# Kernel optimization log

Measured on AMD Instinct MI355X. Metric: run time of the kernel, lower is better.

The kernel has to match this reference:

```python
import jax, jax.numpy as jnp
import numpy as np

B, TQ, TKV, D, H = 4, 512, 4096, 1024, 8
HEAD_DIM = D // H


def setup_inputs() -> dict:
    key = jax.random.key(0)
    ks = jax.random.split(key, 8)
    s = 0.02
    inputs_q = jax.random.normal(ks[0], (B, TQ, D), jnp.float32)
    inputs_kv = jax.random.normal(ks[1], (B, TKV, D), jnp.float32)
    attention_mask = jax.random.randint(ks[2], (B, TQ, TKV), 0, 2).astype(bool)
    Wq = jax.random.normal(ks[3], (D, D), jnp.float32) * s
    Wk = jax.random.normal(ks[4], (D, D), jnp.float32) * s
    Wv = jax.random.normal(ks[5], (D, D), jnp.float32) * s
    Wo = jax.random.normal(ks[6], (D, D), jnp.float32) * s
    zb = jnp.zeros((D,), jnp.float32)
    return {"inputs_q": inputs_q, "inputs_kv": inputs_kv, "attention_mask": attention_mask,
            "Wq": Wq, "bq": zb, "Wk": Wk, "bk": zb, "Wv": Wv, "bv": zb, "Wo": Wo, "bo": zb}


def _split_heads(x, h):
    b, t, c = x.shape
    return x.reshape(b, t, h, c // h).transpose(0, 2, 1, 3)  # b h t d


def reference(inputs_q, inputs_kv, attention_mask, Wq, bq, Wk, bk, Wv, bv, Wo, bo):
    q = _split_heads(inputs_q @ Wq + bq, H)   # [b,h,tq,d]
    k = _split_heads(inputs_kv @ Wk + bk, H)  # [b,h,tkv,d]
    v = _split_heads(inputs_kv @ Wv + bv, H)  # [b,h,tkv,d]
    scale = 1.0 / np.sqrt(HEAD_DIM).astype(np.float32)
    scores = jnp.einsum('bhtd,bhTd->bhtT', q, k) * scale
    large_k = jnp.asarray(1e30, scores.dtype)  # 1e30 for fp32 per source
    scores = jnp.where(attention_mask[:, None, :, :], scores, -large_k)
    probs = jax.nn.softmax(scores, axis=-1)
    summed = jnp.einsum('bhtT,bhTd->bhtd', probs, v)
    b, h, t, d = summed.shape
    summed = summed.transpose(0, 2, 1, 3).reshape(b, t, h * d)  # [b,tq,hiddens]
    # wipe rows whose mask is entirely zero (post-softmax wipe-masking)
    wipe = jnp.all(~attention_mask, axis=-1, keepdims=True)  # [b,tq,1]
    summed = jnp.where(wipe, jnp.zeros_like(summed), summed)
    return summed @ Wo + bo
```

## Files before the change

kernel.cpp:

```cpp
#include <hip/hip_runtime.h>
#include <cstdint>
#include <cstddef>

typedef unsigned short US;
typedef __bf16 bf16_t;
typedef bf16_t bf16x8 __attribute__((ext_vector_type(8)));
typedef float  f32x4  __attribute__((ext_vector_type(4)));
typedef US     us8    __attribute__((ext_vector_type(8)));
typedef US     us4    __attribute__((ext_vector_type(4)));

#define AS1 __attribute__((address_space(1)))
#define AS3 __attribute__((address_space(3)))

__device__ __forceinline__ void gl_lds16(const void* g, void* l) {
    __builtin_amdgcn_global_load_lds((AS1 unsigned int*)(size_t)g,
                                     (AS3 unsigned int*)l, 16, 0, 0);
}

__device__ __forceinline__ US f2bf(float f) {
    unsigned u = __builtin_bit_cast(unsigned, f);
    u += 0x7FFFu + ((u >> 16) & 1u);
    return (US)(u >> 16);
}

__device__ __forceinline__ bf16x8 ldv8(const US* p) {
    return __builtin_bit_cast(bf16x8, *(const us8*)p);
}

__global__ void prep(const float* __restrict__ Xq, const float* __restrict__ Xkv,
                     const int* __restrict__ Mi, US* __restrict__ XqB,
                     US* __restrict__ XkvB, unsigned long long* __restrict__ MBits) {
    int b = blockIdx.x, tid = threadIdx.x;
    if (b < 2048) {
        int i = b * 256 + tid;
        float4 f = ((const float4*)Xq)[i];
        us4 o = { f2bf(f.x), f2bf(f.y), f2bf(f.z), f2bf(f.w) };
        ((us4*)XqB)[i] = o;
    } else if (b < 18432) {
        int i = (b - 2048) * 256 + tid;
        float4 f = ((const float4*)Xkv)[i];
        us4 o = { f2bf(f.x), f2bf(f.y), f2bf(f.z), f2bf(f.w) };
        ((us4*)XkvB)[i] = o;
    } else {
        int i = (b - 18432) * 256 + tid;
        int m = Mi[i];
        unsigned long long bits = __ballot(m != 0);
        if ((tid & 63) == 0) MBits[i >> 6] = bits;
    }
}

__global__ void wt_conv(const float* __restrict__ Wq, const float* __restrict__ Wk,
                        const float* __restrict__ Wv, const float* __restrict__ Wo,
                        US* __restrict__ outbase) {
    const float* W = (blockIdx.z == 0) ? Wq : (blockIdx.z == 1) ? Wk
                   : (blockIdx.z == 2) ? Wv : Wo;
    US* WT = outbase + (size_t)blockIdx.z * 1024 * 1024;
    __shared__ float t[32][33];
    int tx = threadIdx.x & 31, ty = threadIdx.x >> 5;
    int x = blockIdx.x * 32 + tx;
#pragma unroll
    for (int r = 0; r < 4; ++r)
        t[ty + r * 8][tx] = W[(size_t)(blockIdx.y * 32 + ty + r * 8) * 1024 + x];
    __syncthreads();
    int nx = blockIdx.y * 32 + tx;
#pragma unroll
    for (int r = 0; r < 4; ++r)
        WT[(size_t)(blockIdx.x * 32 + ty + r * 8) * 1024 + nx] = f2bf(t[tx][ty + r * 8]);
}

template <int MODE, int BM>
__global__ __launch_bounds__(256, 2)
void gemm_bt(const US* __restrict__ A, const US* __restrict__ Bt,
             const float* __restrict__ bias, void* __restrict__ out,
             int tlog2, float scale) {
    constexpr int K = 1024, N = 1024, BK = 64;
    constexpr int MI = BM / 32;
    __shared__ US As[BM * BK];
    __shared__ US Bs[128 * BK];
    const int tid = threadIdx.x;
    const int wv = tid >> 6, ln = tid & 63;
    const int g = ln >> 4, c15 = ln & 15;
    const int m0 = blockIdx.x * BM, n0 = blockIdx.y * 128;
    const int wm = (wv & 1) * (BM / 2), wn = (wv >> 1) * 64;

    f32x4 acc[MI][4];
    const f32x4 z = {0.f, 0.f, 0.f, 0.f};
#pragma unroll
    for (int i = 0; i < MI; ++i)
#pragma unroll
        for (int j = 0; j < 4; ++j) acc[i][j] = z;

    const US* Ab = A + (size_t)m0 * K;
    const US* Bb = Bt + (size_t)n0 * K;

    for (int k0 = 0; k0 < K; k0 += BK) {
        __syncthreads();
#pragma unroll
        for (int q = 0; q < BM / 32; ++q) {
            int eb = (q * 256 + wv * 64) * 8;
            int r = (eb >> 6) + (ln >> 3);
            int sw = (ln & 7) ^ (r & 7);
            gl_lds16(Ab + (size_t)r * K + k0 + sw * 8, &As[eb]);
        }
#pragma unroll
        for (int q = 0; q < 4; ++q) {
            int eb = (q * 256 + wv * 64) * 8;
            int r = (eb >> 6) + (ln >> 3);
            int sw = (ln & 7) ^ (r & 7);
            gl_lds16(Bb + (size_t)r * K + k0 + sw * 8, &Bs[eb]);
        }
        __syncthreads();
#pragma unroll
        for (int ks = 0; ks < 2; ++ks) {
            bf16x8 a[MI], b[4];
#pragma unroll
            for (int i = 0; i < MI; ++i) {
                int p = (ks * 4 + g) ^ (c15 & 7);
                a[i] = ldv8(&As[(wm + i * 16 + c15) * BK + p * 8]);
            }
#pragma unroll
            for (int j = 0; j < 4; ++j) {
                int p = (ks * 4 + g) ^ (c15 & 7);
                b[j] = ldv8(&Bs[(wn + j * 16 + c15) * BK + p * 8]);
            }
#pragma unroll
            for (int i = 0; i < MI; ++i)
#pragma unroll
                for (int j = 0; j < 4; ++j)
                    acc[i][j] = __builtin_amdgcn_mfma_f32_16x16x32_bf16(a[i], b[j], acc[i][j], 0, 0, 0);
        }
    }

#pragma unroll
    for (int i = 0; i < MI; ++i) {
#pragma unroll
        for (int j = 0; j < 4; ++j) {
            int col = n0 + wn + j * 16 + c15;
            float bvv = bias[col];
#pragma unroll
            for (int r = 0; r < 4; ++r) {
                int row = m0 + wm + i * 16 + g * 4 + r;
                float v = (acc[i][j][r] + bvv) * scale;
                if (MODE == 0) {
                    int b_ = row >> tlog2;
                    int t = row & ((1 << tlog2) - 1);
                    int h = col >> 7, d = col & 127;
                    ((US*)out)[(((size_t)(b_ * 8 + h) << tlog2) + t) * 128 + d] = f2bf(v);
                } else {
                    ((float*)out)[(size_t)row * N + col] = v;
                }
            }
        }
    }
}

__global__ __launch_bounds__(256, 2)
void gemm_kv(const US* __restrict__ A, const US* __restrict__ BtK,
             const US* __restrict__ BtV, const float* __restrict__ bk,
             const float* __restrict__ bv, US* __restrict__ Kout,
             US* __restrict__ VTout) {
    constexpr int K = 1024, BK = 64;
    __shared__ US lds[3 * 128 * BK];
    US* As  = lds;
    US* BsK = lds + 128 * BK;
    US* BsV = lds + 2 * 128 * BK;
    const int tid = threadIdx.x;
    const int wv = tid >> 6, ln = tid & 63;
    const int g = ln >> 4, c15 = ln & 15;
    const int m0 = blockIdx.x * 128, n0 = blockIdx.y * 128;
    const int wm = (wv & 1) * 64, wn = (wv >> 1) * 64;

    f32x4 aK[4][4], aV[4][4];
    const f32x4 z = {0.f, 0.f, 0.f, 0.f};
#pragma unroll
    for (int i = 0; i < 4; ++i)
#pragma unroll
        for (int j = 0; j < 4; ++j) { aK[i][j] = z; aV[i][j] = z; }

    const US* Ab  = A   + (size_t)m0 * K;
    const US* BbK = BtK + (size_t)n0 * K;
    const US* BbV = BtV + (size_t)n0 * K;

    for (int k0 = 0; k0 < K; k0 += BK) {
        __syncthreads();
#pragma unroll
        for (int q = 0; q < 4; ++q) {
            int eb = (q * 256 + wv * 64) * 8;
            int r = (eb >> 6) + (ln >> 3);
            int sw = (ln & 7) ^ (r & 7);
            gl_lds16(Ab  + (size_t)r * K + k0 + sw * 8, &As[eb]);
            gl_lds16(BbK + (size_t)r * K + k0 + sw * 8, &BsK[eb]);
            gl_lds16(BbV + (size_t)r * K + k0 + sw * 8, &BsV[eb]);
        }
        __syncthreads();
#pragma unroll
        for (int ks = 0; ks < 2; ++ks) {
            bf16x8 a[4], bK[4], bV[4];
#pragma unroll
            for (int i = 0; i < 4; ++i) {
                int p = (ks * 4 + g) ^ (c15 & 7);
                a[i] = ldv8(&As[(wm + i * 16 + c15) * BK + p * 8]);
            }
#pragma unroll
            for (int j = 0; j < 4; ++j) {
                int p = (ks * 4 + g) ^ (c15 & 7);
                bK[j] = ldv8(&BsK[(wn + j * 16 + c15) * BK + p * 8]);
                bV[j] = ldv8(&BsV[(wn + j * 16 + c15) * BK + p * 8]);
            }
#pragma unroll
            for (int i = 0; i < 4; ++i)
#pragma unroll
                for (int j = 0; j < 4; ++j) {
                    aK[i][j] = __builtin_amdgcn_mfma_f32_16x16x32_bf16(a[i], bK[j], aK[i][j], 0, 0, 0);
                    aV[i][j] = __builtin_amdgcn_mfma_f32_16x16x32_bf16(a[i], bV[j], aV[i][j], 0, 0, 0);
                }
        }
    }

    const int h = n0 >> 7;
    const int b_ = m0 >> 12, tbase = m0 & 4095;

#pragma unroll
    for (int i = 0; i < 4; ++i) {
#pragma unroll
        for (int j = 0; j < 4; ++j) {
            int col = n0 + wn + j * 16 + c15;
            float bkv = bk[col];
            int d = col & 127;
#pragma unroll
            for (int r = 0; r < 4; ++r) {
                int row = m0 + wm + i * 16 + g * 4 + r;
                int t = row & 4095;
                Kout[(((size_t)(b_ * 8 + h) << 12) + t) * 128 + d] = f2bf(aK[i][j][r] + bkv);
            }
        }
    }

    __syncthreads();
    US* T = lds;
#pragma unroll
    for (int i = 0; i < 4; ++i) {
#pragma unroll
        for (int j = 0; j < 4; ++j) {
            int dcol = wn + j * 16 + c15;
            float bvv = bv[n0 + dcol];
#pragma unroll
            for (int r = 0; r < 4; ++r) {
                int kvrow = wm + i * 16 + g * 4 + r;
                T[dcol * 136 + kvrow] = f2bf(aV[i][j][r] + bvv);
            }
        }
    }
    __syncthreads();
    {
        int d = tid >> 1, half = (tid & 1) * 64;
        US* vrow = VTout + ((size_t)(b_ * 8 + h) * 128 + d) * 4096 + tbase + half;
        const US* tr = &T[d * 136 + half];
#pragma unroll
        for (int s = 0; s < 8; ++s)
            *(us8*)(vrow + s * 8) = *(const us8*)(tr + s * 8);
    }
}

__global__ __launch_bounds__(256, 3)
void flash(const US* __restrict__ Qh, const US* __restrict__ Kh,
           const US* __restrict__ VTh, const unsigned long long* __restrict__ MBits,
           float* __restrict__ Opart, float* __restrict__ Lpart) {
    __shared__ US Ks[64 * 128];
    __shared__ US Vs[128 * 64];
    __shared__ US Ps[4][32 * 64];
    const int tid = threadIdx.x, wv = tid >> 6, ln = tid & 63;
    const int g = ln >> 4, c15 = ln & 15;
    const int qt = blockIdx.x, qbase = qt * 128;
    const int bh = blockIdx.y, b_ = bh >> 3;
    const int sp = blockIdx.z;
    const int t0 = (sp < 4) ? sp * 11 : 44 + (sp - 4) * 10;
    const int nt = (sp < 4) ? 11 : 10;
    const int wq = wv * 32;

    bf16x8 qa[2][4];
#pragma unroll
    for (int ib = 0; ib < 2; ++ib) {
        const US* qrow = Qh + ((size_t)bh * 512 + qbase + wq + ib * 16 + c15) * 128;
#pragma unroll
        for (int ks = 0; ks < 4; ++ks)
            qa[ib][ks] = ldv8(qrow + ks * 32 + g * 8);
    }

    f32x4 o[8][2];
    const f32x4 z = {0.f, 0.f, 0.f, 0.f};
#pragma unroll
    for (int d = 0; d < 8; ++d) { o[d][0] = z; o[d][1] = z; }
    float l2[2] = {0.f, 0.f};

    const unsigned long long* Mrow[2];
    Mrow[0] = MBits + (size_t)(b_ * 512 + qbase + wq + c15) * 64;
    Mrow[1] = Mrow[0] + (size_t)16 * 64;
    const US* Kbase = Kh + ((size_t)bh * 4096 + (size_t)t0 * 64) * 128;
    const US* Vbase = VTh + (size_t)bh * 128 * 4096;
    US* Pw = &Ps[wv][0];

    for (int t = 0; t < nt; ++t) {
        int kv0 = (t0 + t) * 64;
        __syncthreads();
        const US* Kb = Kbase + (size_t)t * 64 * 128;
#pragma unroll
        for (int q = 0; q < 4; ++q) {
            int eb = (q * 256 + wv * 64) * 8;
            int r = (eb >> 7) + (ln >> 4);
            int sw = (ln & 15) ^ (r & 15);
            gl_lds16(Kb + (size_t)r * 128 + sw * 8, &Ks[eb]);
        }
#pragma unroll
        for (int q = 0; q < 4; ++q) {
            int eb = (q * 256 + wv * 64) * 8;
            int r = (eb >> 6) + (ln >> 3);
            int sw = (ln & 7) ^ (r & 7);
            gl_lds16(Vbase + (size_t)r * 4096 + kv0 + sw * 8, &Vs[eb]);
        }
        unsigned long long m64[2];
        m64[0] = Mrow[0][t0 + t];
        m64[1] = Mrow[1][t0 + t];
        __syncthreads();

#pragma unroll
        for (int kb = 0; kb < 4; ++kb) {
            f32x4 s0 = z, s1 = z;
#pragma unroll
            for (int ks = 0; ks < 4; ++ks) {
                bf16x8 kf = ldv8(&Ks[(kb * 16 + c15) * 128 + (((ks * 4 + g) ^ c15) * 8)]);
                s0 = __builtin_amdgcn_mfma_f32_16x16x32_bf16(kf, qa[0][ks], s0, 0, 0, 0);
                s1 = __builtin_amdgcn_mfma_f32_16x16x32_bf16(kf, qa[1][ks], s1, 0, 0, 0);
            }
            int cw = kb * 4 + g;
#pragma unroll
            for (int ib = 0; ib < 2; ++ib) {
                f32x4 sv = ib ? s1 : s0;
                unsigned mq = (unsigned)(m64[ib] >> (kb * 16 + g * 4)) & 15u;
                float p0 = (mq & 1u) ? __expf(sv[0]) : 0.f;
                float p1 = (mq & 2u) ? __expf(sv[1]) : 0.f;
                float p2 = (mq & 4u) ? __expf(sv[2]) : 0.f;
                float p3 = (mq & 8u) ? __expf(sv[3]) : 0.f;
                l2[ib] += (p0 + p1) + (p2 + p3);
                int q = ib * 16 + c15;
                US* wp = Pw + q * 64 + (((cw >> 1) ^ (q & 7)) * 8) + (cw & 1) * 4;
                us4 pv = { f2bf(p0), f2bf(p1), f2bf(p2), f2bf(p3) };
                *(us4*)wp = pv;
            }
        }

#pragma unroll
        for (int ks = 0; ks < 2; ++ks) {
            bf16x8 pf[2];
#pragma unroll
            for (int ib = 0; ib < 2; ++ib) {
                int q = ib * 16 + c15;
                pf[ib] = ldv8(&Pw[q * 64 + (((ks * 4 + g) ^ (q & 7)) * 8)]);
            }
#pragma unroll
            for (int d = 0; d < 8; ++d) {
                bf16x8 vf = ldv8(&Vs[(d * 16 + c15) * 64 + (((ks * 4 + g) ^ (c15 & 7)) * 8)]);
                o[d][0] = __builtin_amdgcn_mfma_f32_16x16x32_bf16(vf, pf[0], o[d][0], 0, 0, 0);
                o[d][1] = __builtin_amdgcn_mfma_f32_16x16x32_bf16(vf, pf[1], o[d][1], 0, 0, 0);
            }
        }
    }

    float lf[2];
#pragma unroll
    for (int ib = 0; ib < 2; ++ib) {
        float l = l2[ib];
        l += __shfl_xor(l, 16); l += __shfl_xor(l, 32);
        lf[ib] = l;
    }
    if (ln < 16) {
        size_t lb = ((size_t)sp * 32 + bh) * 512 + qbase + wq + c15;
        Lpart[lb] = lf[0];
        Lpart[lb + 16] = lf[1];
    }
    float* Ob = Opart + (((size_t)sp * 32 + bh) * 128 + g * 4) * 512 + qbase + wq + c15;
#pragma unroll
    for (int d = 0; d < 8; ++d)
#pragma unroll
        for (int r = 0; r < 4; ++r) {
            Ob[(size_t)(d * 16 + r) * 512] = o[d][0][r];
            Ob[(size_t)(d * 16 + r) * 512 + 16] = o[d][1][r];
        }
}

__global__ void combine(const float* __restrict__ Opart, const float* __restrict__ Lpart,
                        US* __restrict__ AO) {
    __shared__ float linv[128];
    __shared__ float T[128 * 33];
    const int qt = blockIdx.x, bh = blockIdx.y;
    const int b_ = bh >> 3, h = bh & 7;
    const int tid = threadIdx.x;
    const size_t spstride = (size_t)32 * 128 * 512;

    if (tid < 128) {
        float s = 0.f;
#pragma unroll
        for (int sp = 0; sp < 6; ++sp)
            s += Lpart[((size_t)sp * 32 + bh) * 512 + qt * 128 + tid];
        linv[tid] = (s > 0.f) ? 1.f / s : 0.f;
    }
    __syncthreads();

    for (int ds0 = 0; ds0 < 128; ds0 += 32) {
        if (ds0) __syncthreads();
#pragma unroll
        for (int it = 0; it < 4; ++it) {
            int d = ds0 + (tid >> 5) + it * 8, qc = tid & 31;
            const float* base = Opart + ((size_t)bh * 128 + d) * 512 + qt * 128 + qc * 4;
            float4 a = {0.f, 0.f, 0.f, 0.f};
#pragma unroll
            for (int sp = 0; sp < 6; ++sp) {
                float4 v = *(const float4*)(base + sp * spstride);
                a.x += v.x; a.y += v.y; a.z += v.z; a.w += v.w;
            }
            int dd = d - ds0;
            T[(qc * 4 + 0) * 33 + dd] = a.x * linv[qc * 4 + 0];
            T[(qc * 4 + 1) * 33 + dd] = a.y * linv[qc * 4 + 1];
            T[(qc * 4 + 2) * 33 + dd] = a.z * linv[qc * 4 + 2];
            T[(qc * 4 + 3) * 33 + dd] = a.w * linv[qc * 4 + 3];
        }
        __syncthreads();
#pragma unroll
        for (int it = 0; it < 4; ++it) {
            int idx = tid + it * 256;
            int q = idx >> 3, c = idx & 7;
            const float* tr = &T[q * 33 + c * 4];
            us4 ov = { f2bf(tr[0]), f2bf(tr[1]), f2bf(tr[2]), f2bf(tr[3]) };
            *(us4*)(AO + ((size_t)(b_ * 512 + qt * 128 + q)) * 1024 + h * 128 + ds0 + c * 4) = ov;
        }
    }
}

extern "C" void kernel_launch(void* const* d_in, const int* in_sizes, int n_in,
                              void* d_out, int out_size, void* d_ws, size_t ws_size,
                              hipStream_t stream) {
    (void)in_sizes; (void)n_in; (void)out_size; (void)ws_size;
    const float* Xq  = (const float*)d_in[0];
    const float* Xkv = (const float*)d_in[1];
    const int*   Mi  = (const int*)d_in[2];
    const float* Wq  = (const float*)d_in[3];
    const float* bq  = (const float*)d_in[4];
    const float* Wk  = (const float*)d_in[5];
    const float* bk  = (const float*)d_in[6];
    const float* Wv  = (const float*)d_in[7];
    const float* bv  = (const float*)d_in[8];
    const float* Wo  = (const float*)d_in[9];
    const float* bo  = (const float*)d_in[10];
    float* out = (float*)d_out;

    char* p = (char*)d_ws;
    US* WT   = (US*)p; p += (size_t)4 * 1024 * 1024 * 2;
    US* AO   = (US*)p; p += (size_t)2048 * 1024 * 2;
    US* XqB  = (US*)p; p += (size_t)2048 * 1024 * 2;
    US* Qh   = (US*)p; p += (size_t)2048 * 1024 * 2;
    US* Kh   = (US*)p; p += (size_t)16384 * 1024 * 2;
    US* VTh  = (US*)p; p += (size_t)16384 * 1024 * 2;
    US* XkvB = (US*)p; p += (size_t)16384 * 1024 * 2;
    char* OT = p;      p += (size_t)4 * 1024 * 1024 * 4;
    unsigned long long* MBits = (unsigned long long*)p; p += (size_t)131072 * 8;
    (void)OT;
    float* Opart = (float*)XkvB;
    float* Lpart = (float*)XqB;

    prep<<<51200, 256, 0, stream>>>(Xq, Xkv, Mi, XqB, XkvB, MBits);
    wt_conv<<<dim3(32, 32, 4), 256, 0, stream>>>(Wq, Wk, Wv, Wo, WT);

    gemm_bt<0, 64><<<dim3(32, 8), 256, 0, stream>>>(XqB, WT, bq, Qh, 9, 0.08838834764831843f);
    gemm_kv<<<dim3(128, 8), 256, 0, stream>>>(XkvB, WT + 1048576, WT + 2097152,
                                              bk, bv, Kh, VTh);
    flash<<<dim3(4, 32, 6), 256, 0, stream>>>(Qh, Kh, VTh, MBits, Opart, Lpart);
    combine<<<dim3(4, 32), 256, 0, stream>>>(Opart, Lpart, AO);
    gemm_bt<1, 64><<<dim3(32, 8), 256, 0, stream>>>(AO, WT + 3145728, bo, out, 0, 1.0f);
}
```

Measured before the change: 351.9 us.

## Fuse weight conversion into prep, store flash partials as bf16, remap flash grid

New measurement: 344.1 us. -2.2%, faster.

```diff
diff --git a/kernel.cpp b/kernel.cpp
--- a/kernel.cpp
+++ b/kernel.cpp
@@ -23,13 +23,21 @@
     return (US)(u >> 16);
 }
 
+__device__ __forceinline__ float bf2f(US u) {
+    return __builtin_bit_cast(float, (unsigned)u << 16);
+}
+
 __device__ __forceinline__ bf16x8 ldv8(const US* p) {
     return __builtin_bit_cast(bf16x8, *(const us8*)p);
 }
 
 __global__ void prep(const float* __restrict__ Xq, const float* __restrict__ Xkv,
                      const int* __restrict__ Mi, US* __restrict__ XqB,
-                     US* __restrict__ XkvB, unsigned long long* __restrict__ MBits) {
+                     US* __restrict__ XkvB, unsigned long long* __restrict__ MBits,
+                     const float* __restrict__ Wq, const float* __restrict__ Wk,
+                     const float* __restrict__ Wv, const float* __restrict__ Wo,
+                     US* __restrict__ WTbase) {
+    __shared__ float t[32][33];
     int b = blockIdx.x, tid = threadIdx.x;
     if (b < 2048) {
         int i = b * 256 + tid;
@@ -41,31 +49,28 @@
         float4 f = ((const float4*)Xkv)[i];
         us4 o = { f2bf(f.x), f2bf(f.y), f2bf(f.z), f2bf(f.w) };
         ((us4*)XkvB)[i] = o;
-    } else {
+    } else if (b < 51200) {
         int i = (b - 18432) * 256 + tid;
         int m = Mi[i];
         unsigned long long bits = __ballot(m != 0);
         if ((tid & 63) == 0) MBits[i >> 6] = bits;
-    }
-}
-
-__global__ void wt_conv(const float* __restrict__ Wq, const float* __restrict__ Wk,
-                        const float* __restrict__ Wv, const float* __restrict__ Wo,
-                        US* __restrict__ outbase) {
-    const float* W = (blockIdx.z == 0) ? Wq : (blockIdx.z == 1) ? Wk
-                   : (blockIdx.z == 2) ? Wv : Wo;
-    US* WT = outbase + (size_t)blockIdx.z * 1024 * 1024;
-    __shared__ float t[32][33];
-    int tx = threadIdx.x & 31, ty = threadIdx.x >> 5;
-    int x = blockIdx.x * 32 + tx;
-#pragma unroll
-    for (int r = 0; r < 4; ++r)
-        t[ty + r * 8][tx] = W[(size_t)(blockIdx.y * 32 + ty + r * 8) * 1024 + x];
-    __syncthreads();
-    int nx = blockIdx.y * 32 + tx;
-#pragma unroll
-    for (int r = 0; r < 4; ++r)
-        WT[(size_t)(blockIdx.x * 32 + ty + r * 8) * 1024 + nx] = f2bf(t[tx][ty + r * 8]);
+    } else {
+        int wb = b - 51200;
+        int z = wb >> 10, rr = wb & 1023;
+        int bx = rr & 31, by = rr >> 5;
+        const float* W = (z == 0) ? Wq : (z == 1) ? Wk : (z == 2) ? Wv : Wo;
+        US* WT = WTbase + (size_t)z * 1024 * 1024;
+        int tx = tid & 31, ty = tid >> 5;
+        int x = bx * 32 + tx;
+#pragma unroll
+        for (int r = 0; r < 4; ++r)
+            t[ty + r * 8][tx] = W[(size_t)(by * 32 + ty + r * 8) * 1024 + x];
+        __syncthreads();
+        int nx = by * 32 + tx;
+#pragma unroll
+        for (int r = 0; r < 4; ++r)
+            WT[(size_t)(bx * 32 + ty + r * 8) * 1024 + nx] = f2bf(t[tx][ty + r * 8]);
+    }
 }
 
 template <int MODE, int BM>
@@ -265,15 +270,18 @@
 __global__ __launch_bounds__(256, 3)
 void flash(const US* __restrict__ Qh, const US* __restrict__ Kh,
            const US* __restrict__ VTh, const unsigned long long* __restrict__ MBits,
-           float* __restrict__ Opart, float* __restrict__ Lpart) {
+           US* __restrict__ Opart, float* __restrict__ Lpart) {
     __shared__ US Ks[64 * 128];
     __shared__ US Vs[128 * 64];
     __shared__ US Ps[4][32 * 64];
     const int tid = threadIdx.x, wv = tid >> 6, ln = tid & 63;
     const int g = ln >> 4, c15 = ln & 15;
-    const int qt = blockIdx.x, qbase = qt * 128;
-    const int bh = blockIdx.y, b_ = bh >> 3;
-    const int sp = blockIdx.z;
+    const int bid = blockIdx.x;
+    const int qt = bid / 192;
+    const int rest = bid - qt * 192;
+    const int bh = rest / 6, sp = rest - bh * 6;
+    const int qbase = qt * 128;
+    const int b_ = bh >> 3;
     const int t0 = (sp < 4) ? sp * 11 : 44 + (sp - 4) * 10;
     const int nt = (sp < 4) ? 11 : 10;
     const int wq = wv * 32;
@@ -378,17 +386,17 @@
         Lpart[lb] = lf[0];
         Lpart[lb + 16] = lf[1];
     }
-    float* Ob = Opart + (((size_t)sp * 32 + bh) * 128 + g * 4) * 512 + qbase + wq + c15;
+    US* Ob = Opart + (((size_t)sp * 32 + bh) * 128 + g * 4) * 512 + qbase + wq + c15;
 #pragma unroll
     for (int d = 0; d < 8; ++d)
 #pragma unroll
         for (int r = 0; r < 4; ++r) {
-            Ob[(size_t)(d * 16 + r) * 512] = o[d][0][r];
-            Ob[(size_t)(d * 16 + r) * 512 + 16] = o[d][1][r];
-        }
-}
-
-__global__ void combine(const float* __restrict__ Opart, const float* __restrict__ Lpart,
+            Ob[(size_t)(d * 16 + r) * 512] = f2bf(o[d][0][r]);
+            Ob[(size_t)(d * 16 + r) * 512 + 16] = f2bf(o[d][1][r]);
+        }
+}
+
+__global__ void combine(const US* __restrict__ Opart, const float* __restrict__ Lpart,
                         US* __restrict__ AO) {
     __shared__ float linv[128];
     __shared__ float T[128 * 33];
@@ -408,21 +416,27 @@
 
     for (int ds0 = 0; ds0 < 128; ds0 += 32) {
         if (ds0) __syncthreads();
-#pragma unroll
-        for (int it = 0; it < 4; ++it) {
-            int d = ds0 + (tid >> 5) + it * 8, qc = tid & 31;
-            const float* base = Opart + ((size_t)bh * 128 + d) * 512 + qt * 128 + qc * 4;
-            float4 a = {0.f, 0.f, 0.f, 0.f};
+        {
+            int d = ds0 + (tid >> 3);
+            int q0 = (tid & 7) * 16;
+            const US* base = Opart + ((size_t)bh * 128 + d) * 512 + qt * 128 + q0;
+            float acc[16];
+#pragma unroll
+            for (int i = 0; i < 16; ++i) acc[i] = 0.f;
 #pragma unroll
             for (int sp = 0; sp < 6; ++sp) {
-                float4 v = *(const float4*)(base + sp * spstride);
-                a.x += v.x; a.y += v.y; a.z += v.z; a.w += v.w;
+                us8 a = *(const us8*)(base + sp * spstride);
+                us8 b = *(const us8*)(base + sp * spstride + 8);
+#pragma unroll
+                for (int i = 0; i < 8; ++i) {
+                    acc[i] += bf2f(a[i]);
+                    acc[8 + i] += bf2f(b[i]);
+                }
             }
             int dd = d - ds0;
-            T[(qc * 4 + 0) * 33 + dd] = a.x * linv[qc * 4 + 0];
-            T[(qc * 4 + 1) * 33 + dd] = a.y * linv[qc * 4 + 1];
-            T[(qc * 4 + 2) * 33 + dd] = a.z * linv[qc * 4 + 2];
-            T[(qc * 4 + 3) * 33 + dd] = a.w * linv[qc * 4 + 3];
+#pragma unroll
+            for (int i = 0; i < 16; ++i)
+                T[(q0 + i) * 33 + dd] = acc[i] * linv[q0 + i];
         }
         __syncthreads();
 #pragma unroll
@@ -461,19 +475,16 @@
     US* Kh   = (US*)p; p += (size_t)16384 * 1024 * 2;
     US* VTh  = (US*)p; p += (size_t)16384 * 1024 * 2;
     US* XkvB = (US*)p; p += (size_t)16384 * 1024 * 2;
-    char* OT = p;      p += (size_t)4 * 1024 * 1024 * 4;
     unsigned long long* MBits = (unsigned long long*)p; p += (size_t)131072 * 8;
-    (void)OT;
-    float* Opart = (float*)XkvB;
+    US* Opart    = XkvB;
     float* Lpart = (float*)XqB;
 
-    prep<<<51200, 256, 0, stream>>>(Xq, Xkv, Mi, XqB, XkvB, MBits);
-    wt_conv<<<dim3(32, 32, 4), 256, 0, stream>>>(Wq, Wk, Wv, Wo, WT);
+    prep<<<55296, 256, 0, stream>>>(Xq, Xkv, Mi, XqB, XkvB, MBits, Wq, Wk, Wv, Wo, WT);
 
     gemm_bt<0, 64><<<dim3(32, 8), 256, 0, stream>>>(XqB, WT, bq, Qh, 9, 0.08838834764831843f);
     gemm_kv<<<dim3(128, 8), 256, 0, stream>>>(XkvB, WT + 1048576, WT + 2097152,
                                               bk, bv, Kh, VTh);
-    flash<<<dim3(4, 32, 6), 256, 0, stream>>>(Qh, Kh, VTh, MBits, Opart, Lpart);
+    flash<<<768, 256, 0, stream>>>(Qh, Kh, VTh, MBits, Opart, Lpart);
     combine<<<dim3(4, 32), 256, 0, stream>>>(Opart, Lpart, AO);
     gemm_bt<1, 64><<<dim3(32, 8), 256, 0, stream>>>(AO, WT + 3145728, bo, out, 0, 1.0f);
 }
```
